# Kernel optimization log

Measured on AMD Instinct MI355X. Metric: run time of the kernel, lower is better.

Reference implementation:

```python
import jax, jax.numpy as jnp
import numpy as np

IN_F = 256
OUT_F = 256
H = 4
DH = OUT_F // H  # 64
N = 6144


def setup_inputs() -> dict:
    key = jax.random.key(0)
    ks = jax.random.split(key, 6)
    x = jax.random.normal(ks[0], (N, IN_F), dtype=jnp.float32)
    adj = jax.random.randint(ks[1], (N, N), 0, 2, dtype=jnp.int32)
    # per-head Linear(in_features, d_head): weights [H, IN_F, DH], bias [H, DH]
    W = jax.random.normal(ks[2], (H, IN_F, DH), dtype=jnp.float32) / np.sqrt(IN_F)
    Wb = jax.random.normal(ks[3], (H, DH), dtype=jnp.float32) * 0.01
    # per-head Linear(2*d_head, 1): weights [H, 2*DH], bias [H]
    A = jax.random.normal(ks[4], (H, 2 * DH), dtype=jnp.float32) / np.sqrt(2 * DH)
    Ab = jax.random.normal(ks[5], (H,), dtype=jnp.float32) * 0.01
    return {"x": x, "adj": adj, "W": W, "Wb": Wb, "A": A, "Ab": Ab}


def reference(x, adj, W, Wb, A, Ab):
    # h[h,n,d] = per-head linear projection of node features
    h = jnp.einsum("ni,hid->hnd", x, W) + Wb[:, None, :]
    a_src, a_dst = A[:, :DH], A[:, DH:]
    # score(i,j) = a_src . h_i + a_dst . h_j + b  (decomposed concat-linear)
    s_src = jnp.einsum("hnd,hd->hn", h, a_src) + Ab[:, None]  # [H, N]
    s_dst = jnp.einsum("hnd,hd->hn", h, a_dst)                # [H, N]
    scores = s_src[:, :, None] + s_dst[:, None, :]            # [H, N, N]
    # Faithful to source: non-edges get score 0.0 (not -inf) before softmax
    scores = jnp.where(adj[None, :, :] > 0, scores, 0.0)
    probs = jax.nn.softmax(scores, axis=-1)                   # row softmax
    out = jnp.einsum("hij,hjd->hid", probs, h)                # [H, N, DH]
    # concat heads along feature dim -> [N, H*DH]
    return jnp.transpose(out, (1, 0, 2)).reshape(N, H * DH)
```

## Files before the change

### kernel.cpp

```cpp
#include <hip/hip_runtime.h>
#include <stdint.h>

#define NN 6144
#define NC 576

typedef float f32x4 __attribute__((ext_vector_type(4)));
typedef __bf16 bf16x8v __attribute__((ext_vector_type(8)));

__device__ __forceinline__ unsigned short f2bf(float f) {
  unsigned u = __float_as_uint(f);
  u += 0x7FFFu + ((u >> 16) & 1u);
  return (unsigned short)(u >> 16);
}

__device__ __forceinline__ unsigned char f2e4m3(float f) {
  unsigned u = __float_as_uint(f);
  unsigned sgn = (u >> 24) & 0x80u;
  unsigned au = u & 0x7FFFFFFFu;
  if (au >= 0x43E00000u) return (unsigned char)(sgn | 0x7E);
  if (au < 0x3C800000u) {
    int q = (int)rintf(__uint_as_float(au) * 512.0f);
    return (unsigned char)(sgn | (q >= 8 ? 0x08 : q));
  }
  unsigned r = au + 0x7FFFFu + ((au >> 20) & 1u);
  int e = (int)(r >> 23) - 127;
  unsigned m = (r >> 20) & 7u;
  return (unsigned char)(sgn | ((unsigned)(e + 7) << 3) | m);
}

__device__ __forceinline__ unsigned short pack2(float a, float b) {
  return (unsigned short)f2e4m3(a) | ((unsigned short)f2e4m3(b) << 8);
}

__device__ __forceinline__ void async_load16(const void* g, void* l) {
  __builtin_amdgcn_global_load_lds(
      (__attribute__((address_space(1))) void*)(uintptr_t)g,
      (__attribute__((address_space(3))) void*)(uint32_t)(uintptr_t)l,
      16, 0, 0);
}

__global__ __launch_bounds__(256) void p0s(
    const float* __restrict__ x, const float* __restrict__ W,
    const float* __restrict__ Aw, const float* __restrict__ Wb,
    unsigned short* __restrict__ xsw, unsigned short* __restrict__ wsw,
    float* __restrict__ Acat, float* __restrict__ T)
{
  const int bid = blockIdx.x, t = threadIdx.x;
  if (bid < 8) {
#pragma unroll
    for (int i = 0; i < 4; ++i) {
      const int e = bid * 256 + t + i * 2048;
      const int l = e & 63, kc = (e >> 6) & 7, ct = e >> 9;
      const int c = ct * 16 + (l & 15);
      const int h = c >> 6, d = c & 63;
      const int ks = kc * 32 + (l >> 4) * 8;
      const float* src = W + h * 16384 + ks * 64 + d;
      unsigned uu[4];
#pragma unroll
      for (int j = 0; j < 4; ++j)
        uu[j] = (unsigned)f2bf(src[(2*j) * 64]) | ((unsigned)f2bf(src[(2*j+1) * 64]) << 16);
      *(uint4*)(wsw + (size_t)e * 8) = (uint4){uu[0], uu[1], uu[2], uu[3]};
    }
    return;
  }
  if (bid == 8) {
    T[t] = 0.f;
    const int h = t >> 6, d = t & 63;
    Acat[t]       = Aw[h * 128 + d];
    Acat[256 + t] = Aw[h * 128 + 64 + d];
    Acat[512 + t] = Wb[t];
    return;
  }
  const int tid = (bid - 9) * 256 + t;
#pragma unroll 4
  for (int i = 0; i < 32; ++i) {
    const int e = tid + i * 6144;
    const int l = e & 63, kc = (e >> 6) & 7, mt = e >> 9;
    const int node = mt * 16 + (l & 15);
    const int ks = kc * 32 + (l >> 4) * 8;
    const float4* xp = (const float4*)(x + (size_t)node * 256 + ks);
    float4 v0 = xp[0], v1 = xp[1];
    uint4 o;
    o.x = (unsigned)f2bf(v0.x) | ((unsigned)f2bf(v0.y) << 16);
    o.y = (unsigned)f2bf(v0.z) | ((unsigned)f2bf(v0.w) << 16);
    o.z = (unsigned)f2bf(v1.x) | ((unsigned)f2bf(v1.y) << 16);
    o.w = (unsigned)f2bf(v1.z) | ((unsigned)f2bf(v1.w) << 16);
    *(uint4*)(xsw + (size_t)e * 8) = o;
  }
}

__global__ __launch_bounds__(256) void k1m(
    const unsigned short* __restrict__ xsw, const unsigned short* __restrict__ wsw,
    const float* __restrict__ Acat, const float* __restrict__ Ab,
    const int* __restrict__ adj, unsigned char* __restrict__ A8,
    unsigned char* __restrict__ V8, float* __restrict__ e_src, float* __restrict__ T)
{
  __shared__ unsigned char lv[4][4096];
  __shared__ float lt[256];
  const int t = threadIdx.x;

  if (blockIdx.x >= 192) {
    const int pb = blockIdx.x - 192;
    const int4* a4 = (const int4*)adj;
    unsigned* o1 = (unsigned*)A8;
    const int g0 = pb * 2048 + t;
    int4 q[8];
#pragma unroll
    for (int j = 0; j < 8; ++j) q[j] = a4[g0 + j * 256];
#pragma unroll
    for (int j = 0; j < 8; ++j)
      o1[g0 + j * 256] = (unsigned)q[j].x * 0x38u | (unsigned)q[j].y * 0x3800u |
                         (unsigned)q[j].z * 0x380000u | (unsigned)q[j].w * 0x38000000u;
    return;
  }

  const int w = t >> 6, l = t & 63;
  const int v = blockIdx.x * 4 + w;
  const int mt = v >> 1, nh = v & 1;
  const int i0 = mt * 16, c0 = nh * 128;
  const int lm = l & 15, lk = l >> 4;

  lt[t] = 0.f;
  __syncthreads();

  f32x4 acc[8];
#pragma unroll
  for (int nt = 0; nt < 8; ++nt) acc[nt] = (f32x4){0.f, 0.f, 0.f, 0.f};

  const unsigned short* ap = xsw + ((size_t)mt * 512 + l) * 8;
  const unsigned short* bp = wsw + ((size_t)nh * 4096 + l) * 8;

#pragma unroll
  for (int kc = 0; kc < 8; ++kc) {
    bf16x8v a = *(const bf16x8v*)(ap + (size_t)kc * 512);
#pragma unroll
    for (int nt = 0; nt < 8; ++nt) {
      bf16x8v b = *(const bf16x8v*)(bp + ((size_t)nt * 512 + kc * 64) * 8);
      acc[nt] = __builtin_amdgcn_mfma_f32_16x16x32_bf16(a, b, acc[nt], 0, 0, 0);
    }
  }

  float asv[8], adv[8];
#pragma unroll
  for (int nt = 0; nt < 8; ++nt) {
    const int cc = c0 + nt * 16 + lm;
    const float wb = Acat[512 + cc];
#pragma unroll
    for (int rr = 0; rr < 4; ++rr) acc[nt][rr] += wb;
    asv[nt] = Acat[cc];
    adv[nt] = Acat[256 + cc];
  }

#pragma unroll
  for (int nt = 0; nt < 8; ++nt)
    atomicAdd(&lt[c0 + nt * 16 + lm], acc[nt][0] + acc[nt][1] + acc[nt][2] + acc[nt][3]);

  float ss[2][4], sd[2][4];
#pragma unroll
  for (int hl = 0; hl < 2; ++hl)
#pragma unroll
    for (int rr = 0; rr < 4; ++rr) {
      float s1 = 0.f, s2 = 0.f;
#pragma unroll
      for (int j = 0; j < 4; ++j) {
        s1 += acc[hl * 4 + j][rr] * asv[hl * 4 + j];
        s2 += acc[hl * 4 + j][rr] * adv[hl * 4 + j];
      }
      ss[hl][rr] = s1; sd[hl][rr] = s2;
    }
#pragma unroll
  for (int off = 1; off < 16; off <<= 1)
#pragma unroll
    for (int hl = 0; hl < 2; ++hl)
#pragma unroll
      for (int rr = 0; rr < 4; ++rr) {
        ss[hl][rr] += __shfl_xor(ss[hl][rr], off);
        sd[hl][rr] += __shfl_xor(sd[hl][rr], off);
      }

  float ed[2][4];
#pragma unroll
  for (int hl = 0; hl < 2; ++hl)
#pragma unroll
    for (int rr = 0; rr < 4; ++rr) ed[hl][rr] = expf(sd[hl][rr]);

  if (lm == 0) {
#pragma unroll
    for (int hl = 0; hl < 2; ++hl) {
      const int hh = nh * 2 + hl;
      const float ab = Ab[hh];
#pragma unroll
      for (int rr = 0; rr < 4; ++rr)
        e_src[(size_t)hh * NN + i0 + lk * 4 + rr] = expf(ss[hl][rr] + ab);
    }
  }

  unsigned char* mylv = lv[w];
#pragma unroll
  for (int nt = 0; nt < 8; ++nt) {
    const int hl = nt >> 2;
    const int d = (nt & 3) * 16 + lm;
    const int lcE = hl * 128 + d;
    const int lcP = lcE + 64;
    *(unsigned short*)(mylv + lcE * 16 + lk * 4)     = pack2(ed[hl][0] * acc[nt][0], ed[hl][1] * acc[nt][1]);
    *(unsigned short*)(mylv + lcE * 16 + lk * 4 + 2) = pack2(ed[hl][2] * acc[nt][2], ed[hl][3] * acc[nt][3]);
    *(unsigned short*)(mylv + lcP * 16 + lk * 4)     = pack2(acc[nt][0], acc[nt][1]);
    *(unsigned short*)(mylv + lcP * 16 + lk * 4 + 2) = pack2(acc[nt][2], acc[nt][3]);
  }
#pragma unroll
  for (int j = 0; j < 4; ++j) {
    const int lc = j * 64 + l;
    uint4 val = *(const uint4*)(mylv + lc * 16);
    *(uint4*)(V8 + (size_t)(nh * 256 + lc) * NN + i0) = val;
  }
  if (lm == 0) {
#pragma unroll
    for (int hl = 0; hl < 2; ++hl) {
      const int hh = nh * 2 + hl;
      unsigned char* pq = V8 + (size_t)(512 + hh) * NN + i0 + lk * 4;
      *(unsigned short*)pq       = pack2(ed[hl][0], ed[hl][1]);
      *(unsigned short*)(pq + 2) = pack2(ed[hl][2], ed[hl][3]);
    }
    if (nh == 0)
      *(unsigned*)(V8 + (size_t)516 * NN + i0 + lk * 4) = 0x38383838u;
  }

  __syncthreads();
  atomicAdd(&T[t], lt[t]);
}

__global__ __launch_bounds__(256, 3) void k2_gemm(
    const unsigned char* __restrict__ A8, const unsigned char* __restrict__ V8,
    float* __restrict__ out2, int nks)
{
  __shared__ unsigned char lB[144 * 128];
  const int t   = threadIdx.x;
  const int cb  = blockIdx.x & 3;
  const int rb  = (blockIdx.x >> 2) & 31;
  const int ks  = blockIdx.x >> 7;
  const int krange = NN / nks;
  const int i0 = rb * 192, n0 = cb * 144, k0 = ks * krange;
  const int w = t >> 6, l = t & 63;
  const int lm = l & 15, lk = l >> 4;

  f32x4 acc[3][9];
#pragma unroll
  for (int mt = 0; mt < 3; ++mt)
#pragma unroll
    for (int nt = 0; nt < 9; ++nt) acc[mt][nt] = (f32x4){0.f, 0.f, 0.f, 0.f};

  int scol[5], sgr[5];
#pragma unroll
  for (int u = 0; u < 5; ++u) {
    const int gi = u * 256 + t;
    scol[u] = gi >> 3;
    sgr[u]  = (gi & 7) ^ (scol[u] & 7);
  }
  const int dbase4 = (1024 + (t & ~63)) * 16;

  const unsigned char* gA0 = A8 + (size_t)(i0 + w * 48 + lm) * NN + k0 + lk * 32;
  const unsigned char* gBb = V8 + (size_t)n0 * NN + k0;

  const int iters = krange / 128;
  for (int it = 0; it < iters; ++it) {
    const unsigned char* gB = gBb + it * 128;
#pragma unroll
    for (int u = 0; u < 4; ++u)
      async_load16(gB + (size_t)scol[u] * NN + sgr[u] * 16,
                   (char*)lB + (size_t)(u * 256 + (t & ~63)) * 16);
    if (t < 128)
      async_load16(gB + (size_t)scol[4] * NN + sgr[4] * 16, (char*)lB + dbase4);
    longlong2 afr[3][2];
    const unsigned char* gA = gA0 + it * 128;
#pragma unroll
    for (int mt = 0; mt < 3; ++mt) {
      afr[mt][0] = *(const longlong2*)(gA + (size_t)mt * 16 * NN);
      afr[mt][1] = *(const longlong2*)(gA + (size_t)mt * 16 * NN + 16);
    }
    __syncthreads();
#pragma unroll
    for (int b = 0; b < 2; ++b) {
#pragma unroll
      for (int nt = 0; nt < 9; ++nt) {
        const int cc = nt * 16 + lm;
        const int pos = (lk * 2 + b) ^ (cc & 7);
        longlong2 bv = *(const longlong2*)(lB + cc * 128 + pos * 16);
#pragma unroll
        for (int mt = 0; mt < 3; ++mt) {
          acc[mt][nt] = __builtin_amdgcn_mfma_f32_16x16x32_fp8_fp8(
              afr[mt][b].x, bv.x, acc[mt][nt], 0, 0, 0);
          acc[mt][nt] = __builtin_amdgcn_mfma_f32_16x16x32_fp8_fp8(
              afr[mt][b].y, bv.y, acc[mt][nt], 0, 0, 0);
        }
      }
    }
    __syncthreads();
  }

  float* o = out2 + (size_t)ks * ((size_t)NN * NC);
  const int row0 = i0 + w * 48 + lk * 4;
  const int colb = n0 + lm;
#pragma unroll
  for (int mt = 0; mt < 3; ++mt)
#pragma unroll
    for (int nt = 0; nt < 9; ++nt)
#pragma unroll
      for (int rr = 0; rr < 4; ++rr)
        o[(size_t)(row0 + mt * 16 + rr) * NC + colb + nt * 16] = acc[mt][nt][rr];
}

__global__ __launch_bounds__(256) void k3_final(
    const float* __restrict__ out2, const float* __restrict__ e_src,
    const float* __restrict__ T, float* __restrict__ out, int nks)
{
  const int n = blockIdx.x, c = threadIdx.x;
  const int h = c >> 6, d = c & 63;
  float Se = 0.f, Sp = 0.f, E = 0.f, dg = 0.f;
  for (int s = 0; s < nks; ++s) {
    const float* ra = out2 + (size_t)s * ((size_t)NN * NC) + (size_t)n * NC;
    Se += ra[h * 128 + d];
    Sp += ra[h * 128 + 64 + d];
    E  += ra[512 + h];
    dg += ra[516];
  }
  float e = e_src[h * NN + n];
  float D = e * E + ((float)NN - dg);
  out[(size_t)n * 256 + c] = (e * Se + (T[c] - Sp)) / D;
}

extern "C" void kernel_launch(void* const* d_in, const int* in_sizes, int n_in,
                              void* d_out, int out_size, void* d_ws, size_t ws_size,
                              hipStream_t stream) {
  const float* x  = (const float*)d_in[0];
  const int*   adj= (const int*)d_in[1];
  const float* W  = (const float*)d_in[2];
  const float* Wb = (const float*)d_in[3];
  const float* Aw = (const float*)d_in[4];
  const float* Ab = (const float*)d_in[5];
  float* out = (float*)d_out;
  char* ws = (char*)d_ws;
  unsigned char* V8 = (unsigned char*)ws;
  float* e_src = (float*)(ws + 3538944);
  float* T     = (float*)(ws + 3637248);
  float* Acat  = (float*)(ws + 3638272);
  unsigned short* wsw = (unsigned short*)(ws + 3641344);
  unsigned short* xsw = (unsigned short*)(ws + 3772416);
  unsigned char* A8   = (unsigned char*)(ws + 6918144);
  float* out2  = (float*)(ws + 44666880);

  const size_t slab = (size_t)NN * NC * 4;
  const size_t base = 44666880;
  int nks = 2;
  if (ws_size >= base + 6 * slab)      nks = 6;
  else if (ws_size >= base + 4 * slab) nks = 4;

  hipLaunchKernelGGL(p0s, dim3(33), dim3(256), 0, stream,
                     x, W, Aw, Wb, xsw, wsw, Acat, T);
  hipLaunchKernelGGL(k1m, dim3(4800), dim3(256), 0, stream,
                     xsw, wsw, Acat, Ab, adj, A8, V8, e_src, T);
  hipLaunchKernelGGL(k2_gemm, dim3(128 * nks), dim3(256), 0, stream, A8, V8, out2, nks);
  hipLaunchKernelGGL(k3_final, dim3(NN), dim3(256), 0, stream, out2, e_src, T, out, nks);
}
```

Measured before the change: 307.7 us.

## Fuse adjacency int32-to-fp8 conversion into the attention GEMM A-operand load

Drops the separate pass that converted the int32 adjacency matrix into an fp8 A8 buffer. The GEMM kernel now reads int32 adjacency directly and converts it to fp8 in registers. This removes one full write and read of a 37 MB intermediate. The cost is that the A operand loaded by the GEMM grows 4x (151 MB int32), and it is re-read once per column block (4 times), which adds DRAM/L2 traffic and register pressure in the GEMM.

```diff
diff --git a/kernel.cpp b/kernel.cpp
--- a/kernel.cpp
+++ b/kernel.cpp
@@ -30,6 +30,11 @@
 
 __device__ __forceinline__ unsigned short pack2(float a, float b) {
   return (unsigned short)f2e4m3(a) | ((unsigned short)f2e4m3(b) << 8);
+}
+
+__device__ __forceinline__ unsigned cvt38(int4 q) {
+  return (unsigned)q.x * 0x38u | (unsigned)q.y * 0x3800u |
+         (unsigned)q.z * 0x380000u | (unsigned)q.w * 0x38000000u;
 }
 
 __device__ __forceinline__ void async_load16(const void* g, void* l) {
@@ -89,31 +94,14 @@
   }
 }
 
-__global__ __launch_bounds__(256) void k1m(
+__global__ __launch_bounds__(256) void k1_mfma(
     const unsigned short* __restrict__ xsw, const unsigned short* __restrict__ wsw,
     const float* __restrict__ Acat, const float* __restrict__ Ab,
-    const int* __restrict__ adj, unsigned char* __restrict__ A8,
     unsigned char* __restrict__ V8, float* __restrict__ e_src, float* __restrict__ T)
 {
   __shared__ unsigned char lv[4][4096];
   __shared__ float lt[256];
   const int t = threadIdx.x;
-
-  if (blockIdx.x >= 192) {
-    const int pb = blockIdx.x - 192;
-    const int4* a4 = (const int4*)adj;
-    unsigned* o1 = (unsigned*)A8;
-    const int g0 = pb * 2048 + t;
-    int4 q[8];
-#pragma unroll
-    for (int j = 0; j < 8; ++j) q[j] = a4[g0 + j * 256];
-#pragma unroll
-    for (int j = 0; j < 8; ++j)
-      o1[g0 + j * 256] = (unsigned)q[j].x * 0x38u | (unsigned)q[j].y * 0x3800u |
-                         (unsigned)q[j].z * 0x380000u | (unsigned)q[j].w * 0x38000000u;
-    return;
-  }
-
   const int w = t >> 6, l = t & 63;
   const int v = blockIdx.x * 4 + w;
   const int mt = v >> 1, nh = v & 1;
@@ -230,7 +218,7 @@
 }
 
 __global__ __launch_bounds__(256, 3) void k2_gemm(
-    const unsigned char* __restrict__ A8, const unsigned char* __restrict__ V8,
+    const int* __restrict__ adj, const unsigned char* __restrict__ V8,
     float* __restrict__ out2, int nks)
 {
   __shared__ unsigned char lB[144 * 128];
@@ -258,7 +246,7 @@
   }
   const int dbase4 = (1024 + (t & ~63)) * 16;
 
-  const unsigned char* gA0 = A8 + (size_t)(i0 + w * 48 + lm) * NN + k0 + lk * 32;
+  const int* gA0 = adj + (size_t)(i0 + w * 48 + lm) * NN + k0 + lk * 32;
   const unsigned char* gBb = V8 + (size_t)n0 * NN + k0;
 
   const int iters = krange / 128;
@@ -271,11 +259,17 @@
     if (t < 128)
       async_load16(gB + (size_t)scol[4] * NN + sgr[4] * 16, (char*)lB + dbase4);
     longlong2 afr[3][2];
-    const unsigned char* gA = gA0 + it * 128;
 #pragma unroll
     for (int mt = 0; mt < 3; ++mt) {
-      afr[mt][0] = *(const longlong2*)(gA + (size_t)mt * 16 * NN);
-      afr[mt][1] = *(const longlong2*)(gA + (size_t)mt * 16 * NN + 16);
+      const int4* ap = (const int4*)(gA0 + (size_t)mt * 16 * NN + it * 128);
+      int4 q0 = ap[0], q1 = ap[1], q2 = ap[2], q3 = ap[3];
+      int4 q4 = ap[4], q5 = ap[5], q6 = ap[6], q7 = ap[7];
+      unsigned d0 = cvt38(q0), d1 = cvt38(q1), d2 = cvt38(q2), d3 = cvt38(q3);
+      unsigned d4 = cvt38(q4), d5 = cvt38(q5), d6 = cvt38(q6), d7 = cvt38(q7);
+      afr[mt][0].x = (long)d0 | ((long)d1 << 32);
+      afr[mt][0].y = (long)d2 | ((long)d3 << 32);
+      afr[mt][1].x = (long)d4 | ((long)d5 << 32);
+      afr[mt][1].y = (long)d6 | ((long)d7 << 32);
     }
     __syncthreads();
 #pragma unroll
@@ -345,19 +339,18 @@
   float* Acat  = (float*)(ws + 3638272);
   unsigned short* wsw = (unsigned short*)(ws + 3641344);
   unsigned short* xsw = (unsigned short*)(ws + 3772416);
-  unsigned char* A8   = (unsigned char*)(ws + 6918144);
-  float* out2  = (float*)(ws + 44666880);
+  float* out2  = (float*)(ws + 6918144);
 
   const size_t slab = (size_t)NN * NC * 4;
-  const size_t base = 44666880;
+  const size_t base = 6918144;
   int nks = 2;
   if (ws_size >= base + 6 * slab)      nks = 6;
   else if (ws_size >= base + 4 * slab) nks = 4;
 
   hipLaunchKernelGGL(p0s, dim3(33), dim3(256), 0, stream,
                      x, W, Aw, Wb, xsw, wsw, Acat, T);
-  hipLaunchKernelGGL(k1m, dim3(4800), dim3(256), 0, stream,
-                     xsw, wsw, Acat, Ab, adj, A8, V8, e_src, T);
-  hipLaunchKernelGGL(k2_gemm, dim3(128 * nks), dim3(256), 0, stream, A8, V8, out2, nks);
+  hipLaunchKernelGGL(k1_mfma, dim3(192), dim3(256), 0, stream,
+                     xsw, wsw, Acat, Ab, V8, e_src, T);
+  hipLaunchKernelGGL(k2_gemm, dim3(128 * nks), dim3(256), 0, stream, adj, V8, out2, nks);
   hipLaunchKernelGGL(k3_final, dim3(NN), dim3(256), 0, stream, out2, e_src, T, out, nks);
 }
```

Result: slower. 362.1 us (+17.7%).
